# Performance work log

Measured on AMD Instinct MI355X. Metric: run time of the kernel, lower is better.

## Reference

```python
import jax, jax.numpy as jnp
import numpy as np

C = 32        # channels per degree
NDEG = 4      # degrees 0..3
NLAYERS = 4   # hidden GSE3Res layers
OUTC = 64     # output fiber degree-0 channels
BATCH = 16
NPOINTS = 128
RBF_D = 16


def _sph(u):
    # real spherical harmonics l=0..3 on unit vectors u [E,3]
    x, y, z = u[:, 0], u[:, 1], u[:, 2]
    Y0 = 0.28209479177 * jnp.ones_like(x)[:, None]
    Y1 = 0.48860251190 * jnp.stack([y, z, x], -1)
    Y2 = jnp.stack([1.09254843059 * x * y, 1.09254843059 * y * z,
                    0.31539156525 * (3.0 * z * z - 1.0), 1.09254843059 * x * z,
                    0.54627421529 * (x * x - y * y)], -1)
    Y3 = jnp.stack([0.59004358992 * y * (3.0 * x * x - y * y), 2.89061144264 * x * y * z,
                    0.45704579946 * y * (5.0 * z * z - 1.0), 0.37317633259 * z * (5.0 * z * z - 3.0),
                    0.45704579946 * x * (5.0 * z * z - 1.0), 1.44530572132 * z * (x * x - y * y),
                    0.59004358992 * x * (x * x - 3.0 * y * y)], -1)
    return [Y0, Y1, Y2, Y3]


def _seg_softmax(logits, seg, n):
    m = jax.ops.segment_max(logits, seg, num_segments=n)
    e = jnp.exp(logits - m[seg])
    s = jax.ops.segment_sum(e, seg, num_segments=n)
    return e / s[seg]


def _forward(x, w1, b1, rW, sW, Wv, Wq, Wk, Wo, Wskip, gw, gb,
             w1o, b1o, roW, WvO, WqO, WkO, WoO, WskipO,
             Whid, bhid, Wout, bout, src, dst, gid):
    N = x.shape[0]
    rel = x[dst] - x[src]                                  # [E,3]
    d = jnp.sqrt((rel * rel).sum(-1) + 1e-12)              # [E]
    Ys = _sph(rel / d[:, None])
    centers = jnp.linspace(0.0, 4.0, RBF_D)
    rbf = jnp.exp(-((d[:, None] - centers) ** 2) / (2.0 * 0.5 ** 2))  # [E,16]
    # input fiber {1:1} is zeros_like(x) in the original -> start from zero features
    h = [jnp.zeros((N, C, 2 * l + 1), x.dtype) for l in range(NDEG)]
    for i in range(NLAYERS):
        rh = jax.nn.relu(rbf @ w1[i] + b1[i])              # [E,32] radial net
        q = h[0][:, :, 0] @ Wq[i]                          # [N,32] invariant query
        k = rh @ Wk[i]                                     # [E,32]
        logit = (q[dst] * k).sum(-1) / (C ** 0.5)
        alpha = _seg_softmax(logit, dst, N)
        h0s = h[0][src][:, :, 0]                           # [E,32]
        new = []
        for l in range(NDEG):
            hs = h[l][src]                                 # [E,C,2l+1]
            R = rh @ rW[i, l]                              # [E,C] same-degree radial gate
            S = rh @ sW[i, l]                              # [E,C] degree0->l path
            v = jnp.einsum('ecm,cd->edm', hs, Wv[i, l]) * R[:, :, None]
            v = v + (S * (h0s + 1.0))[:, :, None] * Ys[l][:, None, :]
            agg = jax.ops.segment_sum(alpha[:, None, None] * v, dst, num_segments=N)
            hn = (jnp.einsum('ncm,cd->ndm', h[l], Wskip[i, l])
                  + jnp.einsum('ncm,cd->ndm', agg, Wo[i, l]))
            # GNormBias: norm nonlinearity with learned scale/bias
            nrm = jnp.sqrt((hn * hn).sum(-1) + 1e-12)      # [N,C]
            phi = jax.nn.relu(nrm * gw[i, l] + gb[i, l])
            new.append(hn * (phi / (nrm + 1e-6))[:, :, None])
        h = new
    # final GSE3Res to degree-0 out fiber (64 channels)
    rh = jax.nn.relu(rbf @ w1o + b1o)
    q = h[0][:, :, 0] @ WqO                                # [N,64]
    k = rh @ WkO                                           # [E,64]
    logit = (q[dst] * k).sum(-1) / (OUTC ** 0.5)
    alpha = _seg_softmax(logit, dst, N)
    m0 = jnp.zeros((src.shape[0], OUTC), x.dtype)
    for l in range(NDEG):
        c = jnp.einsum('ecm,em->ec', h[l][src], Ys[l])     # invariant contraction
        m0 = m0 + (c @ WvO[l]) * (rh @ roW[l])
    agg = jax.ops.segment_sum(alpha[:, None] * m0, dst, num_segments=N)
    hout = agg @ WoO + h[0][:, :, 0] @ WskipO              # [N,64]
    # GAvgPooling per graph, then MLP head
    cnt = jax.ops.segment_sum(jnp.ones((N,), x.dtype), gid, num_segments=BATCH)
    pooled = jax.ops.segment_sum(hout, gid, num_segments=BATCH) / cnt[:, None]
    return jax.nn.relu(pooled @ Whid + bhid) @ Wout + bout  # [B,15]


def setup_inputs() -> dict:
    key = jax.random.key(0)
    ks = jax.random.split(key, 30)
    P, B = NPOINTS, BATCH
    N = B * P
    a = np.repeat(np.arange(P), P)
    b = np.tile(np.arange(P), P)
    m = a != b
    a, b = a[m], b[m]
    src = jnp.asarray(np.concatenate([a + g * P for g in range(B)]), jnp.int32)
    dst = jnp.asarray(np.concatenate([b + g * P for g in range(B)]), jnp.int32)
    gid = jnp.asarray(np.repeat(np.arange(B), P), jnp.int32)

    def w(k, shape, s=0.1):
        return (jax.random.normal(k, shape) * s).astype(jnp.float32)

    return {
        'x': jax.random.normal(ks[0], (N, 3), jnp.float32),
        'w1': w(ks[1], (4, 16, 32)), 'b1': w(ks[2], (4, 32)),
        'rW': w(ks[3], (4, 4, 32, 32)), 'sW': w(ks[4], (4, 4, 32, 32)),
        'Wv': w(ks[5], (4, 4, 32, 32)), 'Wq': w(ks[6], (4, 32, 32)), 'Wk': w(ks[7], (4, 32, 32)),
        'Wo': w(ks[8], (4, 4, 32, 32)), 'Wskip': w(ks[9], (4, 4, 32, 32)),
        'gw': w(ks[10], (4, 4, 32)), 'gb': w(ks[11], (4, 4, 32)) + 0.5,
        'w1o': w(ks[12], (16, 32)), 'b1o': w(ks[13], (32,)),
        'roW': w(ks[14], (4, 32, 64)), 'WvO': w(ks[15], (4, 32, 64)),
        'WqO': w(ks[16], (32, 64)), 'WkO': w(ks[17], (32, 64)),
        'WoO': w(ks[18], (64, 64)), 'WskipO': w(ks[19], (32, 64)),
        'Whid': w(ks[20], (64, 64)), 'bhid': w(ks[21], (64,)),
        'Wout': w(ks[22], (64, 15)), 'bout': w(ks[23], (15,)),
        'src': src, 'dst': dst, 'gid': gid,
    }


def reference(x, w1, b1, rW, sW, Wv, Wq, Wk, Wo, Wskip, gw, gb,
              w1o, b1o, roW, WvO, WqO, WkO, WoO, WskipO,
              Whid, bhid, Wout, bout, src, dst, gid):
    return _forward(x, w1, b1, rW, sW, Wv, Wq, Wk, Wo, Wskip, gw, gb,
                    w1o, b1o, roW, WvO, WqO, WkO, WoO, WskipO,
                    Whid, bhid, Wout, bout, src, dst, gid)
```

## Files before the change

kernel.cpp:

```cpp
#include <hip/hip_runtime.h>
#include <hip/hip_bf16.h>
#include <hip/hip_fp16.h>

#define NNODE 2048
#define NGRAPH 16

__device__ __forceinline__ int lmap(int m) { return m == 0 ? 0 : (m < 4 ? 1 : (m < 9 ? 2 : 3)); }

__device__ __forceinline__ float f4get(const float4& v, int j) {
    return j == 0 ? v.x : (j == 1 ? v.y : (j == 2 ? v.z : v.w));
}

__device__ __forceinline__ uint32_t f2h2(float a, float b) {
    __half2 h2 = __floats2half2_rn(a, b);
    return *reinterpret_cast<uint32_t*>(&h2);
}
__device__ __forceinline__ float2 h2f2(uint32_t u) {
    __half2 h2 = *reinterpret_cast<__half2*>(&u);
    return __half22float2(h2);
}

__device__ __forceinline__ void sph16(float x, float y, float z, float* Y) {
    Y[0] = 0.28209479177f;
    Y[1] = 0.4886025119f * y; Y[2] = 0.4886025119f * z; Y[3] = 0.4886025119f * x;
    Y[4] = 1.09254843059f * x * y;
    Y[5] = 1.09254843059f * y * z;
    Y[6] = 0.31539156525f * (3.f * z * z - 1.f);
    Y[7] = 1.09254843059f * x * z;
    Y[8] = 0.54627421529f * (x * x - y * y);
    Y[9]  = 0.59004358992f * y * (3.f * x * x - y * y);
    Y[10] = 2.89061144264f * x * y * z;
    Y[11] = 0.45704579946f * y * (5.f * z * z - 1.f);
    Y[12] = 0.37317633259f * z * (5.f * z * z - 3.f);
    Y[13] = 0.45704579946f * x * (5.f * z * z - 1.f);
    Y[14] = 1.44530572132f * z * (x * x - y * y);
    Y[15] = 0.59004358992f * x * (x * x - 3.f * y * y);
}

#define PROC_SRC(aa, u0, u1, u2, u3, h0v) { \
    int a_ = a0 + (aa); \
    float w_ = alphas[a_]; \
    if (w_ != 0.f) { \
        const float* ysa = &yss[a_ * 17]; \
        float hb1 = (h0v) + 1.f; \
        float sc0 = S[aa][0] * hb1, sc1 = S[aa][1] * hb1; \
        float sc2 = S[aa][2] * hb1, sc3 = S[aa][3] * hb1; \
        acc[0]  = fmaf(w_, fmaf((u0).x, R[aa][0], sc0 * ysa[0]),  acc[0]); \
        acc[1]  = fmaf(w_, fmaf((u0).y, R[aa][1], sc1 * ysa[1]),  acc[1]); \
        acc[2]  = fmaf(w_, fmaf((u0).z, R[aa][1], sc1 * ysa[2]),  acc[2]); \
        acc[3]  = fmaf(w_, fmaf((u0).w, R[aa][1], sc1 * ysa[3]),  acc[3]); \
        acc[4]  = fmaf(w_, fmaf((u1).x, R[aa][2], sc2 * ysa[4]),  acc[4]); \
        acc[5]  = fmaf(w_, fmaf((u1).y, R[aa][2], sc2 * ysa[5]),  acc[5]); \
        acc[6]  = fmaf(w_, fmaf((u1).z, R[aa][2], sc2 * ysa[6]),  acc[6]); \
        acc[7]  = fmaf(w_, fmaf((u1).w, R[aa][2], sc2 * ysa[7]),  acc[7]); \
        acc[8]  = fmaf(w_, fmaf((u2).x, R[aa][2], sc2 * ysa[8]),  acc[8]); \
        acc[9]  = fmaf(w_, fmaf((u2).y, R[aa][3], sc3 * ysa[9]),  acc[9]); \
        acc[10] = fmaf(w_, fmaf((u2).z, R[aa][3], sc3 * ysa[10]), acc[10]); \
        acc[11] = fmaf(w_, fmaf((u2).w, R[aa][3], sc3 * ysa[11]), acc[11]); \
        acc[12] = fmaf(w_, fmaf((u3).x, R[aa][3], sc3 * ysa[12]), acc[12]); \
        acc[13] = fmaf(w_, fmaf((u3).y, R[aa][3], sc3 * ysa[13]), acc[13]); \
        acc[14] = fmaf(w_, fmaf((u3).z, R[aa][3], sc3 * ysa[14]), acc[14]); \
        acc[15] = fmaf(w_, fmaf((u3).w, R[aa][3], sc3 * ysa[15]), acc[15]); \
    } }

__global__ __launch_bounds__(256, 3) void k_layer(
    const float* __restrict__ x, const float* __restrict__ h,
    const float* __restrict__ vpre, const float* __restrict__ wqk,
    const float* __restrict__ w1, const float* __restrict__ b1,
    const float* __restrict__ rW, const float* __restrict__ sW,
    const float* __restrict__ Wskip, const float* __restrict__ Wo,
    const float* __restrict__ gw, const float* __restrict__ gb,
    const float* __restrict__ Wv_n, const float* __restrict__ Wq_n, const float* __restrict__ Wk_n,
    const float* __restrict__ WvO, const float* __restrict__ WqO, const float* __restrict__ WkO,
    float* __restrict__ hnew, float* __restrict__ vpre_n, float* __restrict__ wqk_n,
    float* __restrict__ wq2, float* __restrict__ U,
    int layer, int last)
{
    __shared__ uint32_t rwswP[4096];
    __shared__ __align__(16) float rhs[128 * 36];
    __shared__ __align__(16) float yss[128 * 17];
    __shared__ __align__(16) float ub[1056];
    __shared__ float b1s[32];
    __shared__ float wqks[32];
    __shared__ float alphas[128];
    __shared__ float red[256];
    __shared__ float scale[128];
    __shared__ float sh_inv;

    int n = blockIdx.x, t = threadIdx.x;
    int g = n >> 7, b = n & 127;
    int gbase = g << 7;

    float* xs = ub;
    float* w1s = ub + 384;

    for (int o = t; o < 384; o += 256) xs[o] = x[gbase * 3 + o];
    for (int o = t; o < 512; o += 256) w1s[o] = w1[layer * 512 + o];
    if (t < 32) { b1s[t] = b1[layer * 32 + t]; wqks[t] = wqk[n * 32 + t]; }
    for (int o = t; o < 4096; o += 256)
        rwswP[o] = f2h2(rW[layer * 4096 + o], sW[layer * 4096 + o]);
    __syncthreads();

    {
        int a = t & 127, dh = t >> 7;
        float rx = xs[b * 3 + 0] - xs[a * 3 + 0];
        float ry = xs[b * 3 + 1] - xs[a * 3 + 1];
        float rz = xs[b * 3 + 2] - xs[a * 3 + 2];
        float dd = sqrtf(rx * rx + ry * ry + rz * rz + 1e-12f);
        float inv = 1.f / dd;
        float ys[16];
        sph16(rx * inv, ry * inv, rz * inv, ys);
        if (dh == 0) {
#pragma unroll
            for (int m = 0; m < 16; m++) yss[a * 17 + m] = ys[m];
        }
        float rbf[16];
#pragma unroll
        for (int j = 0; j < 16; j++) {
            float dc = dd - (4.f / 15.f) * j;
            rbf[j] = __expf(-2.f * dc * dc);
        }
        float lpart = 0.f;
        int d0 = dh * 16;
        for (int d2 = 0; d2 < 16; d2++) {
            int d = d0 + d2;
            float s = b1s[d];
#pragma unroll
            for (int j = 0; j < 16; j++) s = fmaf(rbf[j], w1s[j * 32 + d], s);
            s = fmaxf(s, 0.f);
            rhs[a * 36 + d] = s;
            lpart = fmaf(s, wqks[d], lpart);
        }
        red[t] = lpart;
    }
    __syncthreads();
    if (t < 128) alphas[t] = (red[t] + red[t + 128]) * 0.17677669529663687f;
    __syncthreads();

    red[t] = (t < 128 && t != b) ? alphas[t] : -1e30f;
    __syncthreads();
    for (int s2 = 128; s2 > 0; s2 >>= 1) { if (t < s2) red[t] = fmaxf(red[t], red[t + s2]); __syncthreads(); }
    float mx = red[0];
    __syncthreads();
    float e = (t < 128 && t != b) ? __expf(alphas[t] - mx) : 0.f;
    red[t] = e;
    __syncthreads();
    for (int s2 = 128; s2 > 0; s2 >>= 1) { if (t < s2) red[t] += red[t + s2]; __syncthreads(); }
    if (t == 0) sh_inv = 1.f / red[0];
    if (t < 128) alphas[t] = e;
    __syncthreads();

    int grp = t >> 5, d = t & 31;
    float acc[16];
#pragma unroll
    for (int m = 0; m < 16; m++) acc[m] = 0.f;

    for (int chunk = 0; chunk < 2; chunk++) {
        int a0 = grp * 16 + chunk * 8;
        float R[8][4], S[8][4];
#pragma unroll
        for (int aa = 0; aa < 8; aa++)
#pragma unroll
            for (int l = 0; l < 4; l++) { R[aa][l] = 0.f; S[aa][l] = 0.f; }

#pragma unroll 2
        for (int jq = 0; jq < 8; jq++) {
            float4 rh4[8];
#pragma unroll
            for (int aa = 0; aa < 8; aa++)
                rh4[aa] = *reinterpret_cast<const float4*>(&rhs[(a0 + aa) * 36 + jq * 4]);
#pragma unroll
            for (int l = 0; l < 4; l++) {
#pragma unroll
                for (int jj = 0; jj < 4; jj++) {
                    float2 w2 = h2f2(rwswP[(l * 32 + jq * 4 + jj) * 32 + d]);
#pragma unroll
                    for (int aa = 0; aa < 8; aa++) {
                        float rv = f4get(rh4[aa], jj);
                        R[aa][l] = fmaf(rv, w2.x, R[aa][l]);
                        S[aa][l] = fmaf(rv, w2.y, S[aa][l]);
                    }
                }
            }
        }

        float4 A0, A1, A2, A3, B0, B1, B2, B3; float Ah, Bh;
        {
            int nb = (gbase + a0) * 512 + d * 16;
            const float4* p4 = reinterpret_cast<const float4*>(vpre + nb);
            A0 = p4[0]; A1 = p4[1]; A2 = p4[2]; A3 = p4[3]; Ah = h[nb];
            int nb2 = (gbase + a0 + 1) * 512 + d * 16;
            const float4* q4 = reinterpret_cast<const float4*>(vpre + nb2);
            B0 = q4[0]; B1 = q4[1]; B2 = q4[2]; B3 = q4[3]; Bh = h[nb2];
        }
#pragma unroll
        for (int ap = 0; ap < 4; ap++) {
            int aa = ap * 2;
            {
                float4 u0 = A0, u1 = A1, u2 = A2, u3 = A3; float h0v = Ah;
                if (ap < 3) {
                    int nb2 = (gbase + a0 + aa + 2) * 512 + d * 16;
                    const float4* p4 = reinterpret_cast<const float4*>(vpre + nb2);
                    A0 = p4[0]; A1 = p4[1]; A2 = p4[2]; A3 = p4[3]; Ah = h[nb2];
                }
                PROC_SRC(aa, u0, u1, u2, u3, h0v)
            }
            {
                float4 u0 = B0, u1 = B1, u2 = B2, u3 = B3; float h0v = Bh;
                if (ap < 3) {
                    int nb2 = (gbase + a0 + aa + 3) * 512 + d * 16;
                    const float4* p4 = reinterpret_cast<const float4*>(vpre + nb2);
                    B0 = p4[0]; B1 = p4[1]; B2 = p4[2]; B3 = p4[3]; Bh = h[nb2];
                }
                PROC_SRC(aa + 1, u0, u1, u2, u3, h0v)
            }
        }
    }
    __syncthreads();

    float* P = rhs;
#pragma unroll
    for (int m = 0; m < 16; m++) P[grp * 528 + m * 33 + d] = acc[m];
    float* hs = yss;
    for (int o = t; o < 512; o += 256) hs[o] = h[n * 512 + o];
    for (int o = t; o < 4096; o += 256) rwswP[o] = __float_as_uint(Wo[layer * 4096 + o]);
    __syncthreads();

    float* hnS = ub;
    float* aggL = ub + 528;
    float invs = sh_inv;
    for (int o = t; o < 512; o += 256) {
        int m = o >> 5, c = o & 31;
        float s = 0.f;
#pragma unroll
        for (int gg = 0; gg < 8; gg++) s += P[gg * 528 + m * 33 + c];
        aggL[m * 33 + c] = s * invs;
    }
    __syncthreads();

    for (int o = t; o < 4096; o += 256) rhs[o] = Wskip[layer * 4096 + o];
    __syncthreads();

    for (int o = t; o < 512; o += 256) {
        int m = o >> 5, dd = o & 31, l = lmap(m);
        float s = 0.f;
        const float* wa = &rhs[l * 1024 + dd];
        const uint32_t* wb = &rwswP[l * 1024 + dd];
        const float* hrow = &hs[m];
        const float* arow = &aggL[m * 33];
#pragma unroll
        for (int c = 0; c < 32; c++) {
            s = fmaf(hrow[c * 16], wa[c * 32], s);
            s = fmaf(arow[c], __uint_as_float(wb[c * 32]), s);
        }
        hnS[m * 33 + dd] = s;
    }
    __syncthreads();

    if (t < 128) {
        int dd = t >> 2, l = t & 3;
        int m0 = l * l, cnt = 2 * l + 1;
        float s = 1e-12f;
        for (int m = m0; m < m0 + cnt; m++) { float v = hnS[m * 33 + dd]; s = fmaf(v, v, s); }
        float nr = sqrtf(s);
        float phi = fmaxf(nr * gw[(layer * 4 + l) * 32 + dd] + gb[(layer * 4 + l) * 32 + dd], 0.f);
        scale[dd * 4 + l] = phi / (nr + 1e-6f);
    }
    if (!last) {
        for (int o = t; o < 4096; o += 256) rwswP[o] = __float_as_uint(Wv_n[o]);
    } else {
        for (int o = t; o < 4096; o += 256) {
            rhs[o] = WvO[o];
            rwswP[o] = __float_as_uint(WvO[4096 + o]);
        }
    }
    __syncthreads();

    for (int o = t; o < 512; o += 256) {
        int dd = o >> 4, m = o & 15;
        float v = hnS[m * 33 + dd] * scale[dd * 4 + lmap(m)];
        hnew[n * 512 + o] = v;
        hnS[m * 33 + dd] = v;
    }
    __syncthreads();

    if (!last) {
        for (int o = t; o < 512; o += 256) {
            int dd = o >> 4, m = o & 15, l = lmap(m);
            float s = 0.f;
            const uint32_t* wv = &rwswP[l * 1024 + dd];
            const float* hrow = &hnS[m * 33];
#pragma unroll
            for (int c = 0; c < 32; c++) s = fmaf(hrow[c], __uint_as_float(wv[c * 32]), s);
            vpre_n[n * 512 + o] = s;
        }
        if (t < 32) {
            float s = 0.f;
#pragma unroll
            for (int c = 0; c < 32; c++) s = fmaf(hnS[c * 33], Wq_n[c * 32 + t], s);
            red[t] = s;
        }
        __syncthreads();
        if (t < 32) {
            float s = 0.f;
#pragma unroll
            for (int j = 0; j < 32; j++) s = fmaf(Wk_n[t * 32 + j], red[j], s);
            wqk_n[n * 32 + t] = s;
        }
    } else {
        for (int o = t; o < 1024; o += 256) {
            int j = o >> 4, m = o & 15, l = lmap(m);
            float s = 0.f;
            const float* hrow = &hnS[m * 33];
            if (l < 2) {
                const float* wv = &rhs[l * 2048 + j];
#pragma unroll
                for (int c = 0; c < 32; c++) s = fmaf(hrow[c], wv[c * 64], s);
            } else {
                const uint32_t* wv = &rwswP[(l - 2) * 2048 + j];
#pragma unroll
                for (int c = 0; c < 32; c++) s = fmaf(hrow[c], __uint_as_float(wv[c * 64]), s);
            }
            U[n * 1024 + o] = s;
        }
        if (t < 64) {
            float s = 0.f;
#pragma unroll
            for (int c = 0; c < 32; c++) s = fmaf(hnS[c * 33], WqO[c * 64 + t], s);
            red[t] = s;
        }
        __syncthreads();
        if (t < 32) {
            float s = 0.f;
#pragma unroll
            for (int j = 0; j < 64; j++) s = fmaf(WkO[t * 64 + j], red[j], s);
            wq2[n * 32 + t] = s;
        }
    }
}

__global__ __launch_bounds__(256, 3) void k_out_edge(
    const float* __restrict__ x, const float* __restrict__ h,
    const float* __restrict__ w1o, const float* __restrict__ b1o,
    const float* __restrict__ wq2, const float* __restrict__ roW,
    const float* __restrict__ U, const float* __restrict__ WoO,
    const float* __restrict__ WskipO, float* __restrict__ hout)
{
    __shared__ uint32_t rosP[4096];
    __shared__ __align__(16) float rhs[128 * 36];
    __shared__ __align__(16) float yss[128 * 17];
    __shared__ float xs[384];
    __shared__ float w1s[512];
    __shared__ float b1s[32];
    __shared__ float wq2s[32];
    __shared__ float alphas[128];
    __shared__ float red[256];
    __shared__ float agg64s[64];
    __shared__ float sh_inv;

    int n = blockIdx.x, t = threadIdx.x;
    int g = n >> 7, b = n & 127;
    int gbase = g << 7;

    for (int o = t; o < 384; o += 256) xs[o] = x[gbase * 3 + o];
    for (int o = t; o < 512; o += 256) w1s[o] = w1o[o];
    if (t < 32) { b1s[t] = b1o[t]; wq2s[t] = wq2[n * 32 + t]; }
    for (int o = t; o < 4096; o += 256) {
        int j = o & 63, lc = o >> 6, cp = lc & 15, l = lc >> 4;
        rosP[o] = f2h2(roW[(l * 32 + 2 * cp) * 64 + j], roW[(l * 32 + 2 * cp + 1) * 64 + j]);
    }
    __syncthreads();

    {
        int a = t & 127, dh = t >> 7;
        float rx = xs[b * 3 + 0] - xs[a * 3 + 0];
        float ry = xs[b * 3 + 1] - xs[a * 3 + 1];
        float rz = xs[b * 3 + 2] - xs[a * 3 + 2];
        float dd = sqrtf(rx * rx + ry * ry + rz * rz + 1e-12f);
        float inv = 1.f / dd;
        float ys[16];
        sph16(rx * inv, ry * inv, rz * inv, ys);
        if (dh == 0) {
#pragma unroll
            for (int m = 0; m < 16; m++) yss[a * 17 + m] = ys[m];
        }
        float rbf[16];
#pragma unroll
        for (int j = 0; j < 16; j++) {
            float dc = dd - (4.f / 15.f) * j;
            rbf[j] = __expf(-2.f * dc * dc);
        }
        float lpart = 0.f;
        int d0 = dh * 16;
        for (int d2 = 0; d2 < 16; d2++) {
            int d = d0 + d2;
            float s = b1s[d];
#pragma unroll
            for (int j = 0; j < 16; j++) s = fmaf(rbf[j], w1s[j * 32 + d], s);
            s = fmaxf(s, 0.f);
            rhs[a * 36 + d] = s;
            lpart = fmaf(s, wq2s[d], lpart);
        }
        red[t] = lpart;
    }
    __syncthreads();
    if (t < 128) alphas[t] = (red[t] + red[t + 128]) * 0.125f;
    __syncthreads();

    red[t] = (t < 128 && t != b) ? alphas[t] : -1e30f;
    __syncthreads();
    for (int s2 = 128; s2 > 0; s2 >>= 1) { if (t < s2) red[t] = fmaxf(red[t], red[t + s2]); __syncthreads(); }
    float mx = red[0];
    __syncthreads();
    float e = (t < 128 && t != b) ? __expf(alphas[t] - mx) : 0.f;
    red[t] = e;
    __syncthreads();
    for (int s2 = 128; s2 > 0; s2 >>= 1) { if (t < s2) red[t] += red[t + s2]; __syncthreads(); }
    if (t == 0) sh_inv = 1.f / red[0];
    if (t < 128) alphas[t] = e;
    __syncthreads();

    int grp = t >> 6, j = t & 63;
    float accO = 0.f;
    for (int chunk = 0; chunk < 4; chunk++) {
        int a0 = grp * 32 + chunk * 8;
        float RO[8][4];
#pragma unroll
        for (int aa = 0; aa < 8; aa++)
#pragma unroll
            for (int l = 0; l < 4; l++) RO[aa][l] = 0.f;

#pragma unroll 2
        for (int cq = 0; cq < 8; cq++) {
            float4 rh4[8];
#pragma unroll
            for (int aa = 0; aa < 8; aa++)
                rh4[aa] = *reinterpret_cast<const float4*>(&rhs[(a0 + aa) * 36 + cq * 4]);
#pragma unroll
            for (int l = 0; l < 4; l++) {
#pragma unroll
                for (int ch = 0; ch < 2; ch++) {
                    float2 w2 = h2f2(rosP[(l * 16 + cq * 2 + ch) * 64 + j]);
#pragma unroll
                    for (int aa = 0; aa < 8; aa++) {
                        RO[aa][l] = fmaf(f4get(rh4[aa], 2 * ch), w2.x, RO[aa][l]);
                        RO[aa][l] = fmaf(f4get(rh4[aa], 2 * ch + 1), w2.y, RO[aa][l]);
                    }
                }
            }
        }

        float4 A0, A1, A2, A3, B0, B1, B2, B3;
        {
            const float4* p4 = reinterpret_cast<const float4*>(U + (gbase + a0) * 1024 + j * 16);
            A0 = p4[0]; A1 = p4[1]; A2 = p4[2]; A3 = p4[3];
            const float4* q4 = reinterpret_cast<const float4*>(U + (gbase + a0 + 1) * 1024 + j * 16);
            B0 = q4[0]; B1 = q4[1]; B2 = q4[2]; B3 = q4[3];
        }
#define PROC_O(aa, u0, u1, u2, u3) { \
        int a_ = a0 + (aa); \
        float w_ = alphas[a_]; \
        if (w_ != 0.f) { \
            const float* ysa = &yss[a_ * 17]; \
            float cv0 = ysa[0] * (u0).x; \
            float cv1 = fmaf(ysa[1], (u0).y, fmaf(ysa[2], (u0).z, ysa[3] * (u0).w)); \
            float cv2 = fmaf(ysa[4], (u1).x, fmaf(ysa[5], (u1).y, fmaf(ysa[6], (u1).z, fmaf(ysa[7], (u1).w, ysa[8] * (u2).x)))); \
            float cv3 = fmaf(ysa[9], (u2).y, fmaf(ysa[10], (u2).z, fmaf(ysa[11], (u2).w, \
                        fmaf(ysa[12], (u3).x, fmaf(ysa[13], (u3).y, fmaf(ysa[14], (u3).z, ysa[15] * (u3).w)))))); \
            float s_ = fmaf(cv0, RO[aa][0], fmaf(cv1, RO[aa][1], fmaf(cv2, RO[aa][2], cv3 * RO[aa][3]))); \
            accO = fmaf(w_, s_, accO); \
        } }
#pragma unroll
        for (int ap = 0; ap < 4; ap++) {
            int aa = ap * 2;
            {
                float4 u0 = A0, u1 = A1, u2 = A2, u3 = A3;
                if (ap < 3) {
                    const float4* p4 = reinterpret_cast<const float4*>(U + (gbase + a0 + aa + 2) * 1024 + j * 16);
                    A0 = p4[0]; A1 = p4[1]; A2 = p4[2]; A3 = p4[3];
                }
                PROC_O(aa, u0, u1, u2, u3)
            }
            {
                float4 u0 = B0, u1 = B1, u2 = B2, u3 = B3;
                if (ap < 3) {
                    const float4* p4 = reinterpret_cast<const float4*>(U + (gbase + a0 + aa + 3) * 1024 + j * 16);
                    B0 = p4[0]; B1 = p4[1]; B2 = p4[2]; B3 = p4[3];
                }
                PROC_O(aa + 1, u0, u1, u2, u3)
            }
        }
#undef PROC_O
    }
    red[t] = accO;
    __syncthreads();
    if (t < 64) agg64s[t] = (red[t] + red[64 + t] + red[128 + t] + red[192 + t]) * sh_inv;
    __syncthreads();

    if (t < 64) {
        float s = 0.f;
#pragma unroll
        for (int c = 0; c < 64; c++) s = fmaf(agg64s[c], WoO[c * 64 + t], s);
        const float* hr = &h[n * 512];
#pragma unroll
        for (int c = 0; c < 32; c++) s = fmaf(hr[c * 16], WskipO[c * 64 + t], s);
        hout[n * 64 + t] = s;
    }
}

__global__ __launch_bounds__(64) void k_final(
    const float* __restrict__ hout, const float* __restrict__ Whid,
    const float* __restrict__ bhid, const float* __restrict__ Wout,
    const float* __restrict__ bout, float* __restrict__ out)
{
    __shared__ float pooled[64], hid[64];
    int g = blockIdx.x, t = threadIdx.x;
    float s = 0.f;
    for (int p = 0; p < 128; p++) s += hout[(g * 128 + p) * 64 + t];
    pooled[t] = s * (1.f / 128.f);
    __syncthreads();
    float hv = bhid[t];
#pragma unroll
    for (int c = 0; c < 64; c++) hv = fmaf(pooled[c], Whid[c * 64 + t], hv);
    hid[t] = fmaxf(hv, 0.f);
    __syncthreads();
    if (t < 15) {
        float o = bout[t];
#pragma unroll
        for (int c = 0; c < 64; c++) o = fmaf(hid[c], Wout[c * 15 + t], o);
        out[g * 15 + t] = o;
    }
}

extern "C" void kernel_launch(void* const* d_in, const int* in_sizes, int n_in,
                              void* d_out, int out_size, void* d_ws, size_t ws_size,
                              hipStream_t stream) {
    const float* x      = (const float*)d_in[0];
    const float* w1     = (const float*)d_in[1];
    const float* b1     = (const float*)d_in[2];
    const float* rW     = (const float*)d_in[3];
    const float* sW     = (const float*)d_in[4];
    const float* Wv     = (const float*)d_in[5];
    const float* Wq     = (const float*)d_in[6];
    const float* Wk     = (const float*)d_in[7];
    const float* Wo     = (const float*)d_in[8];
    const float* Wskip  = (const float*)d_in[9];
    const float* gw     = (const float*)d_in[10];
    const float* gb     = (const float*)d_in[11];
    const float* w1o    = (const float*)d_in[12];
    const float* b1o    = (const float*)d_in[13];
    const float* roW    = (const float*)d_in[14];
    const float* WvO    = (const float*)d_in[15];
    const float* WqO    = (const float*)d_in[16];
    const float* WkO    = (const float*)d_in[17];
    const float* WoO    = (const float*)d_in[18];
    const float* WskipO = (const float*)d_in[19];
    const float* Whid   = (const float*)d_in[20];
    const float* bhid   = (const float*)d_in[21];
    const float* Wout   = (const float*)d_in[22];
    const float* bout   = (const float*)d_in[23];
    float* out = (float*)d_out;

    float* ws = (float*)d_ws;
    float* h0    = ws;
    float* h1    = h0 + NNODE * 512;
    float* vA    = h1 + NNODE * 512;
    float* wqkA  = vA + NNODE * 512;
    float* vB    = wqkA + NNODE * 32;
    float* wqkB  = vB + NNODE * 512;
    float* wq2   = wqkB + NNODE * 32;
    float* U     = wq2 + NNODE * 32;
    float* hout  = U + NNODE * 1024;

    hipMemsetAsync(h0, 0, NNODE * 512 * sizeof(float), stream);
    hipMemsetAsync(vA, 0, (NNODE * 512 + NNODE * 32) * sizeof(float), stream);

    for (int i = 0; i < 4; i++) {
        const float* hc  = (i & 1) ? h1 : h0;
        float*       hn  = (i & 1) ? h0 : h1;
        const float* vin  = (i & 1) ? vB : vA;
        const float* qin  = (i & 1) ? wqkB : wqkA;
        float*       vout = (i & 1) ? vA : vB;
        float*       qout = (i & 1) ? wqkA : wqkB;
        int last = (i == 3);
        k_layer<<<NNODE, 256, 0, stream>>>(
            x, hc, vin, qin, w1, b1, rW, sW, Wskip, Wo, gw, gb,
            Wv + (last ? 0 : (i + 1) * 4096),
            Wq + (last ? 0 : (i + 1) * 1024),
            Wk + (last ? 0 : (i + 1) * 1024),
            WvO, WqO, WkO,
            hn, vout, qout, wq2, U, i, last);
    }
    k_out_edge<<<NNODE, 256, 0, stream>>>(x, h0, w1o, b1o, wq2, roW, U, WoO, WskipO, hout);
    k_final<<<NGRAPH, 64, 0, stream>>>(hout, Whid, bhid, Wout, bout, out);
}
```

Measured before the change: 601.0 us.

## Swizzle radial weight LDS layout, use wave-shuffle softmax, drop alpha branch

Stores the packed half2 rW/sW weights in shared memory with an XOR-swizzled, per-channel contiguous layout, so each thread loads four weights with one 128-bit LDS read instead of four scalar reads. The tree-based shared-memory softmax reductions, each step followed by a barrier, become wave64 shuffle reductions with only a couple of barriers. The zero-alpha branch in the message accumulation is removed, giving straight-line FMA code at the cost of doing the self-edge work that used to be skipped. The swizzle is meant to avoid LDS bank conflicts for the vector loads.

```diff
diff --git a/kernel.cpp b/kernel.cpp
--- a/kernel.cpp
+++ b/kernel.cpp
@@ -40,28 +40,27 @@
 #define PROC_SRC(aa, u0, u1, u2, u3, h0v) { \
     int a_ = a0 + (aa); \
     float w_ = alphas[a_]; \
-    if (w_ != 0.f) { \
-        const float* ysa = &yss[a_ * 17]; \
-        float hb1 = (h0v) + 1.f; \
-        float sc0 = S[aa][0] * hb1, sc1 = S[aa][1] * hb1; \
-        float sc2 = S[aa][2] * hb1, sc3 = S[aa][3] * hb1; \
-        acc[0]  = fmaf(w_, fmaf((u0).x, R[aa][0], sc0 * ysa[0]),  acc[0]); \
-        acc[1]  = fmaf(w_, fmaf((u0).y, R[aa][1], sc1 * ysa[1]),  acc[1]); \
-        acc[2]  = fmaf(w_, fmaf((u0).z, R[aa][1], sc1 * ysa[2]),  acc[2]); \
-        acc[3]  = fmaf(w_, fmaf((u0).w, R[aa][1], sc1 * ysa[3]),  acc[3]); \
-        acc[4]  = fmaf(w_, fmaf((u1).x, R[aa][2], sc2 * ysa[4]),  acc[4]); \
-        acc[5]  = fmaf(w_, fmaf((u1).y, R[aa][2], sc2 * ysa[5]),  acc[5]); \
-        acc[6]  = fmaf(w_, fmaf((u1).z, R[aa][2], sc2 * ysa[6]),  acc[6]); \
-        acc[7]  = fmaf(w_, fmaf((u1).w, R[aa][2], sc2 * ysa[7]),  acc[7]); \
-        acc[8]  = fmaf(w_, fmaf((u2).x, R[aa][2], sc2 * ysa[8]),  acc[8]); \
-        acc[9]  = fmaf(w_, fmaf((u2).y, R[aa][3], sc3 * ysa[9]),  acc[9]); \
-        acc[10] = fmaf(w_, fmaf((u2).z, R[aa][3], sc3 * ysa[10]), acc[10]); \
-        acc[11] = fmaf(w_, fmaf((u2).w, R[aa][3], sc3 * ysa[11]), acc[11]); \
-        acc[12] = fmaf(w_, fmaf((u3).x, R[aa][3], sc3 * ysa[12]), acc[12]); \
-        acc[13] = fmaf(w_, fmaf((u3).y, R[aa][3], sc3 * ysa[13]), acc[13]); \
-        acc[14] = fmaf(w_, fmaf((u3).z, R[aa][3], sc3 * ysa[14]), acc[14]); \
-        acc[15] = fmaf(w_, fmaf((u3).w, R[aa][3], sc3 * ysa[15]), acc[15]); \
-    } }
+    const float* ysa = &yss[a_ * 17]; \
+    float hb1 = (h0v) + 1.f; \
+    float sc0 = S[aa][0] * hb1, sc1 = S[aa][1] * hb1; \
+    float sc2 = S[aa][2] * hb1, sc3 = S[aa][3] * hb1; \
+    acc[0]  = fmaf(w_, fmaf((u0).x, R[aa][0], sc0 * ysa[0]),  acc[0]); \
+    acc[1]  = fmaf(w_, fmaf((u0).y, R[aa][1], sc1 * ysa[1]),  acc[1]); \
+    acc[2]  = fmaf(w_, fmaf((u0).z, R[aa][1], sc1 * ysa[2]),  acc[2]); \
+    acc[3]  = fmaf(w_, fmaf((u0).w, R[aa][1], sc1 * ysa[3]),  acc[3]); \
+    acc[4]  = fmaf(w_, fmaf((u1).x, R[aa][2], sc2 * ysa[4]),  acc[4]); \
+    acc[5]  = fmaf(w_, fmaf((u1).y, R[aa][2], sc2 * ysa[5]),  acc[5]); \
+    acc[6]  = fmaf(w_, fmaf((u1).z, R[aa][2], sc2 * ysa[6]),  acc[6]); \
+    acc[7]  = fmaf(w_, fmaf((u1).w, R[aa][2], sc2 * ysa[7]),  acc[7]); \
+    acc[8]  = fmaf(w_, fmaf((u2).x, R[aa][2], sc2 * ysa[8]),  acc[8]); \
+    acc[9]  = fmaf(w_, fmaf((u2).y, R[aa][3], sc3 * ysa[9]),  acc[9]); \
+    acc[10] = fmaf(w_, fmaf((u2).z, R[aa][3], sc3 * ysa[10]), acc[10]); \
+    acc[11] = fmaf(w_, fmaf((u2).w, R[aa][3], sc3 * ysa[11]), acc[11]); \
+    acc[12] = fmaf(w_, fmaf((u3).x, R[aa][3], sc3 * ysa[12]), acc[12]); \
+    acc[13] = fmaf(w_, fmaf((u3).y, R[aa][3], sc3 * ysa[13]), acc[13]); \
+    acc[14] = fmaf(w_, fmaf((u3).z, R[aa][3], sc3 * ysa[14]), acc[14]); \
+    acc[15] = fmaf(w_, fmaf((u3).w, R[aa][3], sc3 * ysa[15]), acc[15]); \
+    }
 
 __global__ __launch_bounds__(256, 3) void k_layer(
     const float* __restrict__ x, const float* __restrict__ h,
@@ -76,7 +75,7 @@
     float* __restrict__ wq2, float* __restrict__ U,
     int layer, int last)
 {
-    __shared__ uint32_t rwswP[4096];
+    __shared__ __align__(16) uint32_t rwswP[4096];
     __shared__ __align__(16) float rhs[128 * 36];
     __shared__ __align__(16) float yss[128 * 17];
     __shared__ __align__(16) float ub[1056];
@@ -97,8 +96,12 @@
     for (int o = t; o < 384; o += 256) xs[o] = x[gbase * 3 + o];
     for (int o = t; o < 512; o += 256) w1s[o] = w1[layer * 512 + o];
     if (t < 32) { b1s[t] = b1[layer * 32 + t]; wqks[t] = wqk[n * 32 + t]; }
-    for (int o = t; o < 4096; o += 256)
-        rwswP[o] = f2h2(rW[layer * 4096 + o], sW[layer * 4096 + o]);
+    for (int idx = t; idx < 4096; idx += 256) {
+        int l = idx >> 10, j = (idx >> 5) & 31, d2 = idx & 31;
+        int o = d2 * 128 + ((((l << 3) + (j >> 2)) ^ (d2 & 7)) << 2) + (j & 3);
+        int src = layer * 4096 + l * 1024 + j * 32 + d2;
+        rwswP[o] = f2h2(rW[src], sW[src]);
+    }
     __syncthreads();
 
     {
@@ -137,20 +140,29 @@
     if (t < 128) alphas[t] = (red[t] + red[t + 128]) * 0.17677669529663687f;
     __syncthreads();
 
-    red[t] = (t < 128 && t != b) ? alphas[t] : -1e30f;
-    __syncthreads();
-    for (int s2 = 128; s2 > 0; s2 >>= 1) { if (t < s2) red[t] = fmaxf(red[t], red[t + s2]); __syncthreads(); }
-    float mx = red[0];
-    __syncthreads();
-    float e = (t < 128 && t != b) ? __expf(alphas[t] - mx) : 0.f;
-    red[t] = e;
-    __syncthreads();
-    for (int s2 = 128; s2 > 0; s2 >>= 1) { if (t < s2) red[t] += red[t + s2]; __syncthreads(); }
-    if (t == 0) sh_inv = 1.f / red[0];
-    if (t < 128) alphas[t] = e;
-    __syncthreads();
+    if (t < 128) {
+        float m = (t != b) ? alphas[t] : -1e30f;
+#pragma unroll
+        for (int off = 32; off > 0; off >>= 1) m = fmaxf(m, __shfl_xor(m, off));
+        if ((t & 63) == 0) red[t >> 6] = m;
+    }
+    __syncthreads();
+    {
+        float mx = fmaxf(red[0], red[1]);
+        if (t < 128) {
+            float e = (t != b) ? __expf(alphas[t] - mx) : 0.f;
+            alphas[t] = e;
+            float s = e;
+#pragma unroll
+            for (int off = 32; off > 0; off >>= 1) s += __shfl_xor(s, off);
+            if ((t & 63) == 0) red[2 + (t >> 6)] = s;
+        }
+    }
+    __syncthreads();
+    if (t == 0) sh_inv = 1.f / (red[2] + red[3]);
 
     int grp = t >> 5, d = t & 31;
+    int dbase = d * 128, dx = d & 7;
     float acc[16];
 #pragma unroll
     for (int m = 0; m < 16; m++) acc[m] = 0.f;
@@ -171,9 +183,12 @@
                 rh4[aa] = *reinterpret_cast<const float4*>(&rhs[(a0 + aa) * 36 + jq * 4]);
 #pragma unroll
             for (int l = 0; l < 4; l++) {
+                uint4 wp = *reinterpret_cast<const uint4*>(
+                    &rwswP[dbase + ((((l << 3) + jq) ^ dx) << 2)]);
 #pragma unroll
                 for (int jj = 0; jj < 4; jj++) {
-                    float2 w2 = h2f2(rwswP[(l * 32 + jq * 4 + jj) * 32 + d]);
+                    uint32_t w = jj == 0 ? wp.x : (jj == 1 ? wp.y : (jj == 2 ? wp.z : wp.w));
+                    float2 w2 = h2f2(w);
 #pragma unroll
                     for (int aa = 0; aa < 8; aa++) {
                         float rv = f4get(rh4[aa], jj);
@@ -407,17 +422,26 @@
     if (t < 128) alphas[t] = (red[t] + red[t + 128]) * 0.125f;
     __syncthreads();
 
-    red[t] = (t < 128 && t != b) ? alphas[t] : -1e30f;
-    __syncthreads();
-    for (int s2 = 128; s2 > 0; s2 >>= 1) { if (t < s2) red[t] = fmaxf(red[t], red[t + s2]); __syncthreads(); }
-    float mx = red[0];
-    __syncthreads();
-    float e = (t < 128 && t != b) ? __expf(alphas[t] - mx) : 0.f;
-    red[t] = e;
-    __syncthreads();
-    for (int s2 = 128; s2 > 0; s2 >>= 1) { if (t < s2) red[t] += red[t + s2]; __syncthreads(); }
-    if (t == 0) sh_inv = 1.f / red[0];
-    if (t < 128) alphas[t] = e;
+    if (t < 128) {
+        float m = (t != b) ? alphas[t] : -1e30f;
+#pragma unroll
+        for (int off = 32; off > 0; off >>= 1) m = fmaxf(m, __shfl_xor(m, off));
+        if ((t & 63) == 0) red[t >> 6] = m;
+    }
+    __syncthreads();
+    {
+        float mx = fmaxf(red[0], red[1]);
+        if (t < 128) {
+            float e = (t != b) ? __expf(alphas[t] - mx) : 0.f;
+            alphas[t] = e;
+            float s = e;
+#pragma unroll
+            for (int off = 32; off > 0; off >>= 1) s += __shfl_xor(s, off);
+            if ((t & 63) == 0) red[2 + (t >> 6)] = s;
+        }
+    }
+    __syncthreads();
+    if (t == 0) sh_inv = 1.f / (red[2] + red[3]);
     __syncthreads();
 
     int grp = t >> 6, j = t & 63;
```

Result: slower. 753.4 us (+25.4%).
